# Kernel tuning notes

Hardware: AMD Instinct MI355X
Metric: run time of the kernel (lower is better)

The kernel has to match this reference:

```python
import jax, jax.numpy as jnp
import numpy as np
from jax import lax

B, L_IN, DEC_LEN = 1024, 2048, 64
H = 128            # hidden_size
CARD, EMB = 200, 16  # categorical feature cardinality / embedding dim
VDIM = 4
IN_SIZE = EMB + 1 + 1  # cat-embed + continuous feat (Linear(1,1)) + target value


def setup_inputs() -> dict:
    key = jax.random.key(0)
    k = jax.random.split(key, 19)
    s = 1.0 / np.sqrt(H)  # torch LSTM/Linear default init scale
    u = lambda kk, shape: jax.random.uniform(kk, shape, minval=-s, maxval=s, dtype=jnp.float32)
    return {
        "cat_in": jax.random.randint(k[0], (B, L_IN), 0, CARD, dtype=jnp.int32),
        "cont_in": jax.random.normal(k[1], (B, L_IN, 1), dtype=jnp.float32),
        "X_in": jax.random.normal(k[2], (B, L_IN, 1), dtype=jnp.float32),
        "cat_out": jax.random.randint(k[3], (B, DEC_LEN), 0, CARD, dtype=jnp.int32),
        "cont_out": jax.random.normal(k[4], (B, DEC_LEN, 1), dtype=jnp.float32),
        # learned params
        "emb_table": jax.random.normal(k[5], (CARD, EMB), dtype=jnp.float32) * 0.02,
        "cont_w": jax.random.normal(k[6], (1, 1), dtype=jnp.float32) * 0.5,  # Linear(1,1,bias=False)
        "Wih_e": u(k[7], (4 * H, IN_SIZE)),
        "Whh_e": u(k[8], (4 * H, H)),
        "b_e": u(k[9], (4 * H,)),   # b_ih + b_hh folded together
        "Wih_d": u(k[10], (4 * H, IN_SIZE)),
        "Whh_d": u(k[11], (4 * H, H)),
        "b_d": u(k[12], (4 * H,)),
        "Wm": u(k[13], (1, H)), "bm": u(k[14], (1,)),
        "Ws": u(k[15], (1, H)), "bs": u(k[16], (1,)),
        "Wv": u(k[17], (VDIM, H)), "bv": u(k[18], (VDIM,)),
    }


def _lstm_cell(x, h, c, Wih, Whh, b):
    # torch gate order: i, f, g, o
    gates = x @ Wih.T + h @ Whh.T + b  # [B, 4H]
    i, f, g, o = jnp.split(gates, 4, axis=-1)
    c_new = jax.nn.sigmoid(f) * c + jax.nn.sigmoid(i) * jnp.tanh(g)
    h_new = jax.nn.sigmoid(o) * jnp.tanh(c_new)
    return h_new, c_new


def reference(cat_in, cont_in, X_in, cat_out, cont_out, emb_table, cont_w,
              Wih_e, Whh_e, b_e, Wih_d, Whh_d, b_d, Wm, bm, Ws, bs, Wv, bv):
    w00 = cont_w[0, 0]
    # feature embedding: Embedding for categorical, Linear(1,1,no bias) for continuous
    feats_in_embed = jnp.concatenate([emb_table[cat_in], cont_in * w00], axis=-1)  # [B,L,EMB+1]
    enc_in = jnp.concatenate([feats_in_embed, X_in], axis=-1)                      # [B,L,IN_SIZE]

    h0 = jnp.zeros((X_in.shape[0], H), dtype=X_in.dtype)

    def enc_step(carry, xt):
        h, c = carry
        return _lstm_cell(xt, h, c, Wih_e, Whh_e, b_e), None

    # encoder outputs are unused downstream; only the final (h, c) state matters
    (h, c), _ = lax.scan(enc_step, (h0, h0), jnp.swapaxes(enc_in, 0, 1))

    feats_out_embed = jnp.concatenate([emb_table[cat_out], cont_out * w00], axis=-1)  # [B,D,EMB+1]

    def dec_step(carry, feats_next):
        h, c, x_prev, f_prev = carry
        xt = jnp.concatenate([f_prev, x_prev], axis=-1)  # [B, IN_SIZE]
        h, c = _lstm_cell(xt, h, c, Wih_d, Whh_d, b_d)
        mu = h @ Wm.T + bm                     # [B,1]
        std = jax.nn.softplus(h @ Ws.T + bs)   # [B,1]
        v = h @ Wv.T + bv                      # [B,VDIM]
        return (h, c, mu, feats_next), (mu, std, v)

    init = (h, c, X_in[:, -1, :], feats_in_embed[:, -1, :])
    _, (means, stds, vs) = lax.scan(dec_step, init, jnp.swapaxes(feats_out_embed, 0, 1))
    # [D,B,*] -> [B,D,*]
    return (jnp.swapaxes(means, 0, 1), jnp.swapaxes(stds, 0, 1), jnp.swapaxes(vs, 0, 1))
```

## Files before the change

kernel.cpp:

```cpp
#include <hip/hip_runtime.h>
#include <math.h>

typedef _Float16 half8 __attribute__((ext_vector_type(8)));
typedef _Float16 half2v __attribute__((ext_vector_type(2)));
typedef float float4v __attribute__((ext_vector_type(4)));

constexpr int Lc   = 2048;
constexpr int DECc = 64;
constexpr int Hc   = 128;
constexpr int EMBc = 16;
constexpr int INc  = 18;
constexpr int NBc  = 4;
constexpr int NTc  = 512;
constexpr int KT   = 5;
constexpr int CARD = 200;
constexpr int ZS   = 160;


__device__ __forceinline__ float rcp_(float x) { return __builtin_amdgcn_rcpf(x); }
__device__ __forceinline__ float sigm(float x) { return rcp_(1.0f + __expf(-x)); }
__device__ __forceinline__ float tanh_(float x) { return 2.0f * rcp_(1.0f + __expf(-2.0f * x)) - 1.0f; }
__device__ __forceinline__ float softplus_(float x) { return __logf(1.0f + __expf(x)); }

__device__ __forceinline__ float sel4(float4v v, int q) {
    const float a = (q & 1) ? v[1] : v[0];
    const float b = (q & 1) ? v[3] : v[2];
    return (q & 2) ? b : a;
}

__global__ __launch_bounds__(NTc, 1) void rnnar_kernel(
    const int*   __restrict__ cat_in,  const float* __restrict__ cont_in,
    const float* __restrict__ X_in,    const int*   __restrict__ cat_out,
    const float* __restrict__ cont_out,const float* __restrict__ emb_table,
    const float* __restrict__ cont_w,
    const float* __restrict__ Wih_e, const float* __restrict__ Whh_e, const float* __restrict__ b_e,
    const float* __restrict__ Wih_d, const float* __restrict__ Whh_d, const float* __restrict__ b_d,
    const float* __restrict__ Wm, const float* __restrict__ bm,
    const float* __restrict__ Ws, const float* __restrict__ bs,
    const float* __restrict__ Wv, const float* __restrict__ bv,
    float* __restrict__ out)
{
    __shared__ _Float16      z_lds[2][NBc * ZS];
    __shared__ _Float16      emb_lds[CARD * EMBc];
    __shared__ _Float16      xs04[Lc * NBc];
    __shared__ _Float16      xs14[Lc * NBc];
    __shared__ unsigned char catb4[Lc * NBc];
    __shared__ _Float16      xo4[DECc * NBc];
    __shared__ unsigned char catob4[DECc * NBc];
    __shared__ float         h32_lds[NBc * 132];
    __shared__ float         wh_lds[6 * Hc];
    __shared__ float         hb_lds[8];

    const int tid  = threadIdx.x;
    const int lane = tid & 63;
    const int wv   = tid >> 6;
    const int q    = lane >> 4;
    const int col  = lane & 15;
    const int cell = 16 * wv + col;
    const int bx   = col & 3;
    const int b0   = blockIdx.x * NBc;
    const float w00 = cont_w[0];

    const int wsub = tid & 3;
    const int wxb  = tid >> 2;

    {
        int* z32 = (int*)&z_lds[0][0];
        for (int i = tid; i < NBc * ZS; i += NTc) z32[i] = 0;
    }
    for (int i = tid; i < CARD * EMBc; i += NTc) emb_lds[i] = (_Float16)emb_table[i];
    for (int i = tid; i < Lc * NBc; i += NTc) {
        const int b = i >> 11, t = i & (Lc - 1);
        catb4[t * 4 + b] = (unsigned char)cat_in[(b0 + b) * Lc + t];
        xs04[t * 4 + b]  = (_Float16)(cont_in[(b0 + b) * Lc + t] * w00);
        xs14[t * 4 + b]  = (_Float16)(X_in[(b0 + b) * Lc + t]);
    }
    if (tid < NBc * DECc) {
        const int b = tid >> 6, t = tid & 63;
        catob4[t * 4 + b] = (unsigned char)cat_out[(b0 + b) * DECc + t];
        xo4[t * 4 + b]    = (_Float16)(cont_out[(b0 + b) * DECc + t] * w00);
    }
    for (int i = tid; i < 6 * Hc; i += NTc) {
        const int o = i >> 7, k = i & 127;
        wh_lds[i] = (o == 0) ? Wm[k] : (o == 1) ? Ws[k] : Wv[(o - 2) * Hc + k];
    }
    if (tid == 0) { hb_lds[0] = bm[0]; hb_lds[1] = bs[0]; }
    if (tid < 4)  { hb_lds[2 + tid] = bv[tid]; }

    half8 Bf[4][KT];
    float bias_s[4];
    #define LOAD_T(WIH, WHH, BB)                                               \
    {                                                                          \
        _Pragma("unroll")                                                      \
        for (int gt = 0; gt < 4; ++gt) {                                       \
            const int row = gt * Hc + cell;                                    \
            _Pragma("unroll")                                                  \
            for (int kt = 0; kt < KT; ++kt) {                                  \
                half8 f;                                                       \
                _Pragma("unroll")                                              \
                for (int j = 0; j < 8; ++j) {                                  \
                    const int k = 32 * kt + 8 * q + j;                         \
                    float v = 0.0f;                                            \
                    if (k < INc)            v = WIH[row * INc + k];            \
                    else if (k < INc + Hc)  v = WHH[row * Hc + (k - INc)];     \
                    f[j] = (_Float16)v;                                        \
                }                                                              \
                Bf[gt][kt] = f;                                                \
            }                                                                  \
            bias_s[gt] = BB[row];                                              \
        }                                                                      \
    }

    LOAD_T(Wih_e, Whh_e, b_e);
    float4v bias4[4];
    #pragma unroll
    for (int gt = 0; gt < 4; ++gt)
        bias4[gt] = (float4v){bias_s[gt], bias_s[gt], bias_s[gt], bias_s[gt]};
    __syncthreads();

    if (tid < 16) {
        if (wsub < 2) {
            const int c4 = (int)catb4[0 * 4 + wxb];
            const half8 e8 = *(const half8*)&emb_lds[c4 * EMBc + 8 * wsub];
            *(half8*)(&z_lds[0][0] + wxb * ZS + 8 * wsub) = e8;
        } else if (wsub == 2) {
            half2v two; two[0] = xs04[0 * 4 + wxb]; two[1] = xs14[0 * 4 + wxb];
            *(half2v*)(&z_lds[0][0] + wxb * ZS + 16) = two;
        }
    }
    __syncthreads();

    int p = 0;
    float c_reg = 0.f;

    for (int t = 0; t < Lc; ++t) {
        const _Float16* zr = &z_lds[p][0];
        _Float16*       zw = &z_lds[p ^ 1][0];
        const int t1 = (t + 1 < Lc) ? t + 1 : Lc - 1;

        int c4n = 0;
        if (tid < 16 && wsub < 2) c4n = (int)catb4[t1 * 4 + wxb];

        const _Float16* ap = zr + bx * ZS + 8 * q;
        half8 Az[KT];
        #pragma unroll
        for (int kt = 0; kt < KT; ++kt) Az[kt] = *(const half8*)(ap + 32 * kt);

        float4v acc[4];
        #pragma unroll
        for (int gt = 0; gt < 4; ++gt) {
            float4v a = bias4[gt];
            #pragma unroll
            for (int kt = 0; kt < KT; ++kt)
                a = __builtin_amdgcn_mfma_f32_16x16x32_f16(Az[kt], Bf[gt][kt], a, 0, 0, 0);
            acc[gt] = a;
        }

        const float gi = sel4(acc[0], q);
        const float gf = sel4(acc[1], q);
        const float gg = sel4(acc[2], q);
        const float go = sel4(acc[3], q);

        const float cn = sigm(gf) * c_reg + sigm(gi) * tanh_(gg);
        c_reg = cn;
        zw[q * ZS + INc + cell] = (_Float16)(sigm(go) * tanh_(cn));

        if (tid < 16) {
            if (wsub < 2) {
                const half8 e8 = *(const half8*)&emb_lds[c4n * EMBc + 8 * wsub];
                *(half8*)(zw + wxb * ZS + 8 * wsub) = e8;
            } else if (wsub == 2) {
                half2v two; two[0] = xs04[t1 * 4 + wxb]; two[1] = xs14[t1 * 4 + wxb];
                *(half2v*)(zw + wxb * ZS + 16) = two;
            }
        }

        __syncthreads();
        p ^= 1;
    }

    LOAD_T(Wih_d, Whh_d, b_d);
    #pragma unroll
    for (int gt = 0; gt < 4; ++gt)
        bias4[gt] = (float4v){bias_s[gt], bias_s[gt], bias_s[gt], bias_s[gt]};
    const float bm0 = hb_lds[0], bs0 = hb_lds[1];

    for (int t = 0; t < DECc; ++t) {
        const _Float16* zr = &z_lds[p][0];
        _Float16*       zw = &z_lds[p ^ 1][0];

        int c4n = 0;
        if (tid < 16 && wsub < 2) c4n = (int)catob4[t * 4 + wxb];

        const _Float16* ap = zr + bx * ZS + 8 * q;
        half8 Az[KT];
        #pragma unroll
        for (int kt = 0; kt < KT; ++kt) Az[kt] = *(const half8*)(ap + 32 * kt);

        float4v acc[4];
        #pragma unroll
        for (int gt = 0; gt < 4; ++gt) {
            float4v a = bias4[gt];
            #pragma unroll
            for (int kt = 0; kt < KT; ++kt)
                a = __builtin_amdgcn_mfma_f32_16x16x32_f16(Az[kt], Bf[gt][kt], a, 0, 0, 0);
            acc[gt] = a;
        }

        const float gi = sel4(acc[0], q);
        const float gf = sel4(acc[1], q);
        const float gg = sel4(acc[2], q);
        const float go = sel4(acc[3], q);

        const float cn = sigm(gf) * c_reg + sigm(gi) * tanh_(gg);
        c_reg = cn;
        const float hv = sigm(go) * tanh_(cn);
        zw[q * ZS + INc + cell] = (_Float16)hv;
        h32_lds[q * 132 + cell] = hv;

        if (tid < 16) {
            if (wsub < 2) {
                const half8 e8 = *(const half8*)&emb_lds[c4n * EMBc + 8 * wsub];
                *(half8*)(zw + wxb * ZS + 8 * wsub) = e8;
            } else if (wsub == 2) {
                zw[wxb * ZS + 16] = xo4[t * 4 + wxb];
            }
        }

        __syncthreads();

        if (tid < 384) {
            const int grp = tid >> 4;
            const int l16 = tid & 15;
            const int b   = grp & 3, o = grp >> 2;
            float s = 0.0f;
            #pragma unroll
            for (int j = 0; j < 8; ++j) {
                const int k = l16 + 16 * j;
                s += wh_lds[o * Hc + k] * h32_lds[b * 132 + k];
            }
            s += __shfl_xor(s, 1);
            s += __shfl_xor(s, 2);
            s += __shfl_xor(s, 4);
            s += __shfl_xor(s, 8);
            if (l16 == 0) {
                const int gb = b0 + b;
                if (o == 0) {
                    const float mu = s + bm0;
                    out[gb * DECc + t] = mu;
                    zw[b * ZS + (INc - 1)] = (_Float16)mu;
                } else if (o == 1) {
                    out[65536 + gb * DECc + t] = softplus_(s + bs0);
                } else {
                    out[131072 + (gb * DECc + t) * 4 + (o - 2)] = s + hb_lds[2 + (o - 2)];
                }
            }
        }
        __syncthreads();
        p ^= 1;
    }
    #undef LOAD_T
}

extern "C" void kernel_launch(void* const* d_in, const int* in_sizes, int n_in,
                              void* d_out, int out_size, void* d_ws, size_t ws_size,
                              hipStream_t stream) {
    rnnar_kernel<<<1024 / NBc, NTc, 0, stream>>>(
        (const int*)d_in[0],   (const float*)d_in[1],  (const float*)d_in[2],
        (const int*)d_in[3],   (const float*)d_in[4],  (const float*)d_in[5],
        (const float*)d_in[6],
        (const float*)d_in[7], (const float*)d_in[8],  (const float*)d_in[9],
        (const float*)d_in[10],(const float*)d_in[11], (const float*)d_in[12],
        (const float*)d_in[13],(const float*)d_in[14],
        (const float*)d_in[15],(const float*)d_in[16],
        (const float*)d_in[17],(const float*)d_in[18],
        (float*)d_out);
}
```

Before: 1.269 ms.

## Precompute embedding-projected gate table and shrink recurrent MFMA K from 160 to 128

A prep kernel folds the categorical embedding through Wih into a per-category gate contribution table (fp16, 512 gates per category) for encoder and decoder. The main kernel then runs only the recurrent Whh part through MFMA (4 K-tiles instead of 5) and adds the table lookup plus the two scalar input terms in fp32 per thread. This removes one MFMA tile per gate per step and the single-thread-group embedding writes into the shared z buffer. In exchange it adds a global-memory gather per step, which is prefetched one step ahead, plus an extra launch.

```diff
diff --git a/kernel.cpp b/kernel.cpp
--- a/kernel.cpp
+++ b/kernel.cpp
@@ -2,7 +2,7 @@
 #include <math.h>
 
 typedef _Float16 half8 __attribute__((ext_vector_type(8)));
-typedef _Float16 half2v __attribute__((ext_vector_type(2)));
+typedef _Float16 half4v __attribute__((ext_vector_type(4)));
 typedef float float4v __attribute__((ext_vector_type(4)));
 
 constexpr int Lc   = 2048;
@@ -12,9 +12,10 @@
 constexpr int INc  = 18;
 constexpr int NBc  = 4;
 constexpr int NTc  = 512;
-constexpr int KT   = 5;
+constexpr int KT   = 4;
 constexpr int CARD = 200;
 constexpr int ZS   = 160;
+constexpr int TBL  = CARD * 512;
 
 
 __device__ __forceinline__ float rcp_(float x) { return __builtin_amdgcn_rcpf(x); }
@@ -26,6 +27,27 @@
     const float a = (q & 1) ? v[1] : v[0];
     const float b = (q & 1) ? v[3] : v[2];
     return (q & 2) ? b : a;
+}
+
+__global__ __launch_bounds__(512, 1) void prep_kernel(
+    const float* __restrict__ emb_table,
+    const float* __restrict__ Wih_e, const float* __restrict__ Wih_d,
+    _Float16* __restrict__ ws)
+{
+    const int c = blockIdx.x;
+    const int g = threadIdx.x;
+    __shared__ float e[EMBc];
+    if (threadIdx.x < EMBc) e[threadIdx.x] = emb_table[c * EMBc + threadIdx.x];
+    __syncthreads();
+    float s0 = 0.f, s1 = 0.f;
+    #pragma unroll
+    for (int k = 0; k < EMBc; ++k) {
+        s0 += e[k] * Wih_e[g * INc + k];
+        s1 += e[k] * Wih_d[g * INc + k];
+    }
+    const int cell = g & 127, gt = g >> 7;
+    ws[c * 512 + cell * 4 + gt]       = (_Float16)s0;
+    ws[TBL + c * 512 + cell * 4 + gt] = (_Float16)s1;
 }
 
 __global__ __launch_bounds__(NTc, 1) void rnnar_kernel(
@@ -38,10 +60,10 @@
     const float* __restrict__ Wm, const float* __restrict__ bm,
     const float* __restrict__ Ws, const float* __restrict__ bs,
     const float* __restrict__ Wv, const float* __restrict__ bv,
+    const _Float16* __restrict__ xtab,
     float* __restrict__ out)
 {
     __shared__ _Float16      z_lds[2][NBc * ZS];
-    __shared__ _Float16      emb_lds[CARD * EMBc];
     __shared__ _Float16      xs04[Lc * NBc];
     __shared__ _Float16      xs14[Lc * NBc];
     __shared__ unsigned char catb4[Lc * NBc];
@@ -50,6 +72,7 @@
     __shared__ float         h32_lds[NBc * 132];
     __shared__ float         wh_lds[6 * Hc];
     __shared__ float         hb_lds[8];
+    __shared__ float         mu_lds[4];
 
     const int tid  = threadIdx.x;
     const int lane = tid & 63;
@@ -61,14 +84,10 @@
     const int b0   = blockIdx.x * NBc;
     const float w00 = cont_w[0];
 
-    const int wsub = tid & 3;
-    const int wxb  = tid >> 2;
-
     {
         int* z32 = (int*)&z_lds[0][0];
         for (int i = tid; i < NBc * ZS; i += NTc) z32[i] = 0;
     }
-    for (int i = tid; i < CARD * EMBc; i += NTc) emb_lds[i] = (_Float16)emb_table[i];
     for (int i = tid; i < Lc * NBc; i += NTc) {
         const int b = i >> 11, t = i & (Lc - 1);
         catb4[t * 4 + b] = (unsigned char)cat_in[(b0 + b) * Lc + t];
@@ -85,10 +104,11 @@
         wh_lds[i] = (o == 0) ? Wm[k] : (o == 1) ? Ws[k] : Wv[(o - 2) * Hc + k];
     }
     if (tid == 0) { hb_lds[0] = bm[0]; hb_lds[1] = bs[0]; }
-    if (tid < 4)  { hb_lds[2 + tid] = bv[tid]; }
+    if (tid < 4)  { hb_lds[2 + tid] = bv[tid]; mu_lds[tid] = 0.0f; }
 
     half8 Bf[4][KT];
     float bias_s[4];
+    float w16_s[4], w17_s[4];
     #define LOAD_T(WIH, WHH, BB)                                               \
     {                                                                          \
         _Pragma("unroll")                                                      \
@@ -98,16 +118,13 @@
             for (int kt = 0; kt < KT; ++kt) {                                  \
                 half8 f;                                                       \
                 _Pragma("unroll")                                              \
-                for (int j = 0; j < 8; ++j) {                                  \
-                    const int k = 32 * kt + 8 * q + j;                         \
-                    float v = 0.0f;                                            \
-                    if (k < INc)            v = WIH[row * INc + k];            \
-                    else if (k < INc + Hc)  v = WHH[row * Hc + (k - INc)];     \
-                    f[j] = (_Float16)v;                                        \
-                }                                                              \
+                for (int j = 0; j < 8; ++j)                                    \
+                    f[j] = (_Float16)WHH[row * Hc + 32 * kt + 8 * q + j];      \
                 Bf[gt][kt] = f;                                                \
             }                                                                  \
             bias_s[gt] = BB[row];                                              \
+            w16_s[gt]  = WIH[row * INc + 16];                                  \
+            w17_s[gt]  = WIH[row * INc + 17];                                  \
         }                                                                      \
     }
 
@@ -118,17 +135,11 @@
         bias4[gt] = (float4v){bias_s[gt], bias_s[gt], bias_s[gt], bias_s[gt]};
     __syncthreads();
 
-    if (tid < 16) {
-        if (wsub < 2) {
-            const int c4 = (int)catb4[0 * 4 + wxb];
-            const half8 e8 = *(const half8*)&emb_lds[c4 * EMBc + 8 * wsub];
-            *(half8*)(&z_lds[0][0] + wxb * ZS + 8 * wsub) = e8;
-        } else if (wsub == 2) {
-            half2v two; two[0] = xs04[0 * 4 + wxb]; two[1] = xs14[0 * 4 + wxb];
-            *(half2v*)(&z_lds[0][0] + wxb * ZS + 16) = two;
-        }
-    }
-    __syncthreads();
+    half4v xg;
+    {
+        const int c0 = (int)catb4[0 * 4 + q];
+        xg = *(const half4v*)(xtab + c0 * 512 + cell * 4);
+    }
 
     int p = 0;
     float c_reg = 0.f;
@@ -136,10 +147,12 @@
     for (int t = 0; t < Lc; ++t) {
         const _Float16* zr = &z_lds[p][0];
         _Float16*       zw = &z_lds[p ^ 1][0];
-        const int t1 = (t + 1 < Lc) ? t + 1 : Lc - 1;
-
-        int c4n = 0;
-        if (tid < 16 && wsub < 2) c4n = (int)catb4[t1 * 4 + wxb];
+
+        const float cv = (float)xs04[t * 4 + q];
+        const float xv = (float)xs14[t * 4 + q];
+        const int   tn = (t + 1 < Lc) ? t + 1 : Lc - 1;
+        const int   cn = (int)catb4[tn * 4 + q];
+        const half4v xg_n = *(const half4v*)(xtab + cn * 512 + cell * 4);
 
         const _Float16* ap = zr + bx * ZS + 8 * q;
         half8 Az[KT];
@@ -156,25 +169,16 @@
             acc[gt] = a;
         }
 
-        const float gi = sel4(acc[0], q);
-        const float gf = sel4(acc[1], q);
-        const float gg = sel4(acc[2], q);
-        const float go = sel4(acc[3], q);
-
-        const float cn = sigm(gf) * c_reg + sigm(gi) * tanh_(gg);
-        c_reg = cn;
-        zw[q * ZS + INc + cell] = (_Float16)(sigm(go) * tanh_(cn));
-
-        if (tid < 16) {
-            if (wsub < 2) {
-                const half8 e8 = *(const half8*)&emb_lds[c4n * EMBc + 8 * wsub];
-                *(half8*)(zw + wxb * ZS + 8 * wsub) = e8;
-            } else if (wsub == 2) {
-                half2v two; two[0] = xs04[t1 * 4 + wxb]; two[1] = xs14[t1 * 4 + wxb];
-                *(half2v*)(zw + wxb * ZS + 16) = two;
-            }
-        }
-
+        const float gi = sel4(acc[0], q) + (float)xg[0] + cv * w16_s[0] + xv * w17_s[0];
+        const float gf = sel4(acc[1], q) + (float)xg[1] + cv * w16_s[1] + xv * w17_s[1];
+        const float gg = sel4(acc[2], q) + (float)xg[2] + cv * w16_s[2] + xv * w17_s[2];
+        const float go = sel4(acc[3], q) + (float)xg[3] + cv * w16_s[3] + xv * w17_s[3];
+
+        const float cn2 = sigm(gf) * c_reg + sigm(gi) * tanh_(gg);
+        c_reg = cn2;
+        zw[q * ZS + cell] = (_Float16)(sigm(go) * tanh_(cn2));
+
+        xg = xg_n;
         __syncthreads();
         p ^= 1;
     }
@@ -184,13 +188,24 @@
     for (int gt = 0; gt < 4; ++gt)
         bias4[gt] = (float4v){bias_s[gt], bias_s[gt], bias_s[gt], bias_s[gt]};
     const float bm0 = hb_lds[0], bs0 = hb_lds[1];
+    const _Float16* xtabd = xtab + TBL;
+
+    {
+        const int c0 = (int)catb4[(Lc - 1) * 4 + q];
+        xg = *(const half4v*)(xtabd + c0 * 512 + cell * 4);
+    }
+    const float cv0 = (float)xs04[(Lc - 1) * 4 + q];
+    const float sv0 = (float)xs14[(Lc - 1) * 4 + q];
 
     for (int t = 0; t < DECc; ++t) {
         const _Float16* zr = &z_lds[p][0];
         _Float16*       zw = &z_lds[p ^ 1][0];
 
-        int c4n = 0;
-        if (tid < 16 && wsub < 2) c4n = (int)catob4[t * 4 + wxb];
+        const float cv = (t == 0) ? cv0 : (float)xo4[(t - 1) * 4 + q];
+        const float sv = (t == 0) ? sv0 : mu_lds[q];
+
+        const int cn = (int)catob4[t * 4 + q];
+        const half4v xg_n = *(const half4v*)(xtabd + cn * 512 + cell * 4);
 
         const _Float16* ap = zr + bx * ZS + 8 * q;
         half8 Az[KT];
@@ -207,26 +222,18 @@
             acc[gt] = a;
         }
 
-        const float gi = sel4(acc[0], q);
-        const float gf = sel4(acc[1], q);
-        const float gg = sel4(acc[2], q);
-        const float go = sel4(acc[3], q);
-
-        const float cn = sigm(gf) * c_reg + sigm(gi) * tanh_(gg);
-        c_reg = cn;
-        const float hv = sigm(go) * tanh_(cn);
-        zw[q * ZS + INc + cell] = (_Float16)hv;
+        const float gi = sel4(acc[0], q) + (float)xg[0] + cv * w16_s[0] + sv * w17_s[0];
+        const float gf = sel4(acc[1], q) + (float)xg[1] + cv * w16_s[1] + sv * w17_s[1];
+        const float gg = sel4(acc[2], q) + (float)xg[2] + cv * w16_s[2] + sv * w17_s[2];
+        const float go = sel4(acc[3], q) + (float)xg[3] + cv * w16_s[3] + sv * w17_s[3];
+
+        const float cn2 = sigm(gf) * c_reg + sigm(gi) * tanh_(gg);
+        c_reg = cn2;
+        const float hv = sigm(go) * tanh_(cn2);
+        zw[q * ZS + cell] = (_Float16)hv;
         h32_lds[q * 132 + cell] = hv;
 
-        if (tid < 16) {
-            if (wsub < 2) {
-                const half8 e8 = *(const half8*)&emb_lds[c4n * EMBc + 8 * wsub];
-                *(half8*)(zw + wxb * ZS + 8 * wsub) = e8;
-            } else if (wsub == 2) {
-                zw[wxb * ZS + 16] = xo4[t * 4 + wxb];
-            }
-        }
-
+        xg = xg_n;
         __syncthreads();
 
         if (tid < 384) {
@@ -248,7 +255,7 @@
                 if (o == 0) {
                     const float mu = s + bm0;
                     out[gb * DECc + t] = mu;
-                    zw[b * ZS + (INc - 1)] = (_Float16)mu;
+                    mu_lds[b] = mu;
                 } else if (o == 1) {
                     out[65536 + gb * DECc + t] = softplus_(s + bs0);
                 } else {
@@ -265,6 +272,9 @@
 extern "C" void kernel_launch(void* const* d_in, const int* in_sizes, int n_in,
                               void* d_out, int out_size, void* d_ws, size_t ws_size,
                               hipStream_t stream) {
+    _Float16* xtab = (_Float16*)d_ws;
+    prep_kernel<<<CARD, 512, 0, stream>>>(
+        (const float*)d_in[5], (const float*)d_in[7], (const float*)d_in[10], xtab);
     rnnar_kernel<<<1024 / NBc, NTc, 0, stream>>>(
         (const int*)d_in[0],   (const float*)d_in[1],  (const float*)d_in[2],
         (const int*)d_in[3],   (const float*)d_in[4],  (const float*)d_in[5],
@@ -274,5 +284,6 @@
         (const float*)d_in[13],(const float*)d_in[14],
         (const float*)d_in[15],(const float*)d_in[16],
         (const float*)d_in[17],(const float*)d_in[18],
+        xtab,
         (float*)d_out);
 }
```

Measured after the change: 1.265 ms. No clear change (-0.3%).
